# Optimization experiments

Hardware: AMD Instinct MI355X
Metric: run time of the kernel (lower is better)

The kernel has to match this reference:

```python
import jax, jax.numpy as jnp
import numpy as np

N = 262144      # nodes per graph
NC = 65536      # common nodes
D = 256         # feature_dim


def setup_inputs() -> dict:
    key = jax.random.key(0)
    ks = jax.random.split(key, 12)
    h_prop = jax.random.normal(ks[0], (N, D), dtype=jnp.float32)
    h_context = jax.random.normal(ks[1], (N, D), dtype=jnp.float32)
    h_orig = jax.random.normal(ks[2], (NC, D), dtype=jnp.float32)
    # unique indices (torch scatter-assign semantics are only well-defined without dups)
    idx_prop = jnp.sort(jax.random.permutation(ks[3], N)[:NC]).astype(jnp.int64)
    idx_ctx = jnp.sort(jax.random.permutation(ks[4], N)[:NC]).astype(jnp.int64)
    # parameters (xavier-ish scale)
    s = 1.0 / np.sqrt(D)
    w_orig = jax.random.normal(ks[5], (D, D), dtype=jnp.float32) * s
    w_prop = jax.random.normal(ks[6], (D, D), dtype=jnp.float32) * s
    w_ctx = jax.random.normal(ks[7], (D, D), dtype=jnp.float32) * s
    W_fuse = jax.random.normal(ks[8], (D, 3 * D), dtype=jnp.float32) * (1.0 / np.sqrt(3 * D))  # torch Linear weight (out,in)
    b_fuse = jnp.zeros((D,), dtype=jnp.float32)
    bias = jax.random.uniform(ks[9], (D,), dtype=jnp.float32, minval=-s, maxval=s)
    return {
        "h_prop": h_prop, "h_context": h_context,
        "h_original_common_nodes": h_orig,
        "w_orig": w_orig, "w_prop": w_prop, "w_ctx": w_ctx,
        "W_fuse": W_fuse, "b_fuse": b_fuse, "bias": bias,
        "common_node_indices_in_prop": idx_prop,
        "common_node_indices_in_context": idx_ctx,
    }


def reference(h_prop, h_context, h_original_common_nodes,
              w_orig, w_prop, w_ctx, W_fuse, b_fuse, bias,
              common_node_indices_in_prop, common_node_indices_in_context):
    # gather common rows + three small GEMMs  [NC, D]
    t_orig = h_original_common_nodes @ w_orig
    t_prop = h_prop[common_node_indices_in_prop] @ w_prop
    t_ctx = h_context[common_node_indices_in_context] @ w_ctx
    # concat-linear-tanh-bias  [NC, D]
    fused = jnp.concatenate([t_orig, t_prop, t_ctx], axis=1) @ W_fuse.T + b_fuse
    fused = jnp.tanh(fused) + bias
    # scatter update into clones of the full tables
    h_prop_updated = h_prop.at[common_node_indices_in_prop].set(fused)
    h_context_updated = h_context.at[common_node_indices_in_context].set(fused)
    return (h_prop_updated, h_context_updated)
```

## Files before the change

kernel.cpp:

```cpp
#include <hip/hip_runtime.h>
#include <hip/hip_bf16.h>
#include <math.h>

#define NN 262144
#define NCC 65536

typedef __bf16 bf16x8 __attribute__((ext_vector_type(8)));
typedef float f32x4 __attribute__((ext_vector_type(4)));

__global__ __launch_bounds__(256) void k_setup(const float* __restrict__ w_orig,
                                               const float* __restrict__ w_prop,
                                               const float* __restrict__ w_ctx,
                                               const float* __restrict__ W_fuse,
                                               __bf16* __restrict__ Mt,
                                               unsigned char* __restrict__ flags) {
    __shared__ float Wl[64 * 65];
    __shared__ float wl[64 * 65];
    int b = blockIdx.x;
    int t = threadIdx.x;
    if (b >= 48) {
        ((uint4*)flags)[(b - 48) * 256 + t] = make_uint4(0u, 0u, 0u, 0u);
        return;
    }
    int seg = b >> 4, rem = b & 15;
    int ot = rem >> 2, mt = rem & 3;
    const float* wseg = seg == 0 ? w_orig : (seg == 1 ? w_prop : w_ctx);
    int to = (t & 15) * 4, tm = (t >> 4) * 4;
    float acc[4][4] = {};
    for (int kc = 0; kc < 4; ++kc) {
        __syncthreads();
        for (int i = 0; i < 16; ++i) {
            int f = i * 256 + t;
            int row = f >> 6, col = f & 63;
            Wl[row * 65 + col] = W_fuse[(size_t)(ot * 64 + row) * 768 + seg * 256 + kc * 64 + col];
            wl[row * 65 + col] = wseg[(size_t)(mt * 64 + row) * 256 + kc * 64 + col];
        }
        __syncthreads();
        for (int k = 0; k < 64; ++k) {
            float wo[4], wm2[4];
#pragma unroll
            for (int i = 0; i < 4; ++i) wo[i] = Wl[(to + i) * 65 + k];
#pragma unroll
            for (int j = 0; j < 4; ++j) wm2[j] = wl[(tm + j) * 65 + k];
#pragma unroll
            for (int i = 0; i < 4; ++i)
#pragma unroll
                for (int j = 0; j < 4; ++j) acc[i][j] += wo[i] * wm2[j];
        }
    }
    for (int i = 0; i < 4; ++i)
        for (int j = 0; j < 4; ++j) {
            int o = ot * 64 + to + i;
            int g = seg * 256 + mt * 64 + tm + j;
            Mt[(size_t)o * 768 + g] = (__bf16)acc[i][j];
        }
}

__global__ void k_setflags(const int* __restrict__ idxp, const int* __restrict__ idxc,
                           unsigned char* fp, unsigned char* fc) {
    int j = blockIdx.x * blockDim.x + threadIdx.x;
    if (j < NCC) { fp[idxp[j]] = 1; fc[idxc[j]] = 1; }
}

__device__ inline bf16x8 cvt8(f32x4 a, f32x4 b) {
    bf16x8 w;
    w[0] = (__bf16)a[0]; w[1] = (__bf16)a[1]; w[2] = (__bf16)a[2]; w[3] = (__bf16)a[3];
    w[4] = (__bf16)b[0]; w[5] = (__bf16)b[1]; w[6] = (__bf16)b[2]; w[7] = (__bf16)b[3];
    return w;
}

__global__ __launch_bounds__(512, 4) void k_main(const float* __restrict__ hp,
                                                 const float* __restrict__ hc,
                                                 const float* __restrict__ horig,
                                                 const __bf16* __restrict__ Mt,
                                                 const float* __restrict__ bfuse,
                                                 const float* __restrict__ bias,
                                                 const int* __restrict__ idxp,
                                                 const int* __restrict__ idxc,
                                                 const unsigned char* __restrict__ fp,
                                                 const unsigned char* __restrict__ fc,
                                                 float* __restrict__ out0,
                                                 float* __restrict__ out1) {
    __shared__ char smem[40960];
    int bid = blockIdx.x >> 1;
    int t = threadIdx.x;

    if (!(blockIdx.x & 1)) {
        int tbl = bid >= 512;
        const unsigned char* F = tbl ? fc : fp;
        const float* S = tbl ? hc : hp;
        float* D = tbl ? out1 : out0;
        int r0 = (tbl ? bid - 512 : bid) * 512;
#pragma unroll
        for (int g = 0; g < 8; ++g) {
            unsigned char fl[8];
            f32x4 v[8];
#pragma unroll
            for (int i = 0; i < 8; ++i) {
                int gl = (g * 8 + i) * 512 + t;
                fl[i] = F[r0 + (gl >> 6)];
            }
#pragma unroll
            for (int i = 0; i < 8; ++i) {
                int gl = (g * 8 + i) * 512 + t;
                int r = r0 + (gl >> 6), slot = gl & 63;
                v[i] = *(const f32x4*)(S + (size_t)(fl[i] ? 0 : r) * 256 + slot * 4);
            }
#pragma unroll
            for (int i = 0; i < 8; ++i) {
                int gl = (g * 8 + i) * 512 + t;
                int r = r0 + (gl >> 6), slot = gl & 63;
                if (!fl[i]) *(f32x4*)(D + (size_t)r * 256 + slot * 4) = v[i];
            }
        }
        return;
    }

    __bf16* Al = (__bf16*)smem;
    __bf16* Bl = (__bf16*)(smem + 8192);
    int jbase = bid * 64;
    int lane = t & 63, wid = t >> 6;
    int wm = wid >> 2, wn = wid & 3;
    int l15 = lane & 15, lq = lane >> 4;

    int ar = t >> 3, aslot = t & 7;
    int jr = jbase + ar;
    const float* rowp0 = horig + (size_t)jr * 256 + aslot * 8;
    const float* rowp1 = hp + (size_t)idxp[jr] * 256 + aslot * 8;
    const float* rowp2 = hc + (size_t)idxc[jr] * 256 + aslot * 8;

    int bo = t >> 1, bkp = t & 1;
    const __bf16* bsrc = Mt + (size_t)bo * 768 + bkp * 32;

    f32x4 a0[2], a1[2];
    bf16x8 vb[4];
    {
        a0[0] = *(const f32x4*)(rowp0);       a1[0] = *(const f32x4*)(rowp0 + 4);
        a0[1] = *(const f32x4*)(rowp0 + 64);  a1[1] = *(const f32x4*)(rowp0 + 68);
#pragma unroll
        for (int i = 0; i < 4; ++i) vb[i] = *(const bf16x8*)(bsrc + i * 8);
    }

    f32x4 acc[2][4] = {};

#pragma unroll
    for (int c = 0; c < 12; ++c) {
        int s = c & 1;
        __syncthreads();
        *(bf16x8*)&Al[ar * 64 + ((aslot ^ (ar & 7)) << 3)] = cvt8(a0[s], a1[s]);
#pragma unroll
        for (int i = 0; i < 4; ++i) {
            int slot = bkp * 4 + i;
            *(bf16x8*)&Bl[bo * 64 + ((slot ^ (bo & 7)) << 3)] = vb[i];
        }
        if (c < 11) {
#pragma unroll
            for (int i = 0; i < 4; ++i) vb[i] = *(const bf16x8*)(bsrc + (c + 1) * 64 + i * 8);
        }
        if (c < 10) {
            int cn = c + 2;
            int seg = cn >> 2, ko = (cn & 3) * 64;
            const float* sp = (seg == 0 ? rowp0 : (seg == 1 ? rowp1 : rowp2)) + ko;
            a0[s] = *(const f32x4*)(sp);
            a1[s] = *(const f32x4*)(sp + 4);
        }
        __syncthreads();
#pragma unroll
        for (int ks = 0; ks < 2; ++ks) {
            bf16x8 af[2], bfr[4];
            int kslot = ks * 4 + lq;
#pragma unroll
            for (int mi = 0; mi < 2; ++mi) {
                int r = wm * 32 + mi * 16 + l15;
                af[mi] = *(const bf16x8*)&Al[r * 64 + ((kslot ^ (r & 7)) << 3)];
            }
#pragma unroll
            for (int ni = 0; ni < 4; ++ni) {
                int o = wn * 64 + ni * 16 + l15;
                bfr[ni] = *(const bf16x8*)&Bl[o * 64 + ((kslot ^ (o & 7)) << 3)];
            }
#pragma unroll
            for (int mi = 0; mi < 2; ++mi)
#pragma unroll
                for (int ni = 0; ni < 4; ++ni)
                    acc[mi][ni] = __builtin_amdgcn_mfma_f32_16x16x32_bf16(af[mi], bfr[ni], acc[mi][ni], 0, 0, 0);
        }
    }

    float bfv[4], biv[4];
#pragma unroll
    for (int ni = 0; ni < 4; ++ni) {
        int o = wn * 64 + ni * 16 + l15;
        bfv[ni] = bfuse[o];
        biv[ni] = bias[o];
    }
    __syncthreads();
    float* scr = (float*)(smem + 8192 + wid * 4096);
#pragma unroll
    for (int mi = 0; mi < 2; ++mi) {
#pragma unroll
        for (int ni = 0; ni < 4; ++ni)
#pragma unroll
            for (int rr = 0; rr < 4; ++rr) {
                float v = tanhf(acc[mi][ni][rr] + bfv[ni]) + biv[ni];
                scr[(lq * 4 + rr) * 64 + ni * 16 + l15] = v;
            }
#pragma unroll
        for (int rnd = 0; rnd < 4; ++rnd) {
            int rr2 = rnd * 4 + lq;
            int j = jbase + wm * 32 + mi * 16 + rr2;
            int gp = idxp[j], gc = idxc[j];
            f32x4 v = *(const f32x4*)&scr[rr2 * 64 + l15 * 4];
            *(f32x4*)(out0 + (size_t)gp * 256 + wn * 64 + l15 * 4) = v;
            *(f32x4*)(out1 + (size_t)gc * 256 + wn * 64 + l15 * 4) = v;
        }
    }
}

extern "C" void kernel_launch(void* const* d_in, const int* in_sizes, int n_in,
                              void* d_out, int out_size, void* d_ws, size_t ws_size,
                              hipStream_t stream) {
    const float* hp     = (const float*)d_in[0];
    const float* hc     = (const float*)d_in[1];
    const float* horig  = (const float*)d_in[2];
    const float* w_orig = (const float*)d_in[3];
    const float* w_prop = (const float*)d_in[4];
    const float* w_ctx  = (const float*)d_in[5];
    const float* W_fuse = (const float*)d_in[6];
    const float* bfuse  = (const float*)d_in[7];
    const float* bias   = (const float*)d_in[8];
    const int* idxp     = (const int*)d_in[9];
    const int* idxc     = (const int*)d_in[10];
    float* out0 = (float*)d_out;
    float* out1 = out0 + (size_t)NN * 256;

    char* ws = (char*)d_ws;
    __bf16* Mt = (__bf16*)ws;
    unsigned char* fp = (unsigned char*)(ws + 393216);
    unsigned char* fc = fp + NN;

    k_setup<<<176, 256, 0, stream>>>(w_orig, w_prop, w_ctx, W_fuse, Mt, fp);
    k_setflags<<<NCC / 256, 256, 0, stream>>>(idxp, idxc, fp, fc);
    k_main<<<2048, 512, 0, stream>>>(hp, hc, horig, Mt, bfuse, bias,
                                     idxp, idxc, fp, fc, out0, out1);
}
```

Before: 291.0 us.

## Split main kernel into streaming copy pass with bf16 compaction and GEMM pass

Replaces the per-row flag with a rank map, so a first streaming pass reads each table row once. It copies unmarked rows to the output and writes marked rows, converted to bf16, into a compact contiguous buffer. A second GEMM kernel then reads contiguous bf16 rows instead of random fp32 gathers from the large tables, and scatters the results. The aim is to remove the scattered gathers and halve the bytes the GEMM reads. The cost is an extra kernel launch, a serialization point between copy and GEMM, and about 64MB of extra bf16 workspace traffic.

```diff
diff --git a/kernel.cpp b/kernel.cpp
--- a/kernel.cpp
+++ b/kernel.cpp
@@ -6,6 +6,7 @@
 #define NCC 65536
 
 typedef __bf16 bf16x8 __attribute__((ext_vector_type(8)));
+typedef __bf16 bf16x4 __attribute__((ext_vector_type(4)));
 typedef float f32x4 __attribute__((ext_vector_type(4)));
 
 __global__ __launch_bounds__(256) void k_setup(const float* __restrict__ w_orig,
@@ -13,13 +14,13 @@
                                                const float* __restrict__ w_ctx,
                                                const float* __restrict__ W_fuse,
                                                __bf16* __restrict__ Mt,
-                                               unsigned char* __restrict__ flags) {
+                                               int* __restrict__ ranks) {
     __shared__ float Wl[64 * 65];
     __shared__ float wl[64 * 65];
     int b = blockIdx.x;
     int t = threadIdx.x;
     if (b >= 48) {
-        ((uint4*)flags)[(b - 48) * 256 + t] = make_uint4(0u, 0u, 0u, 0u);
+        ((uint4*)ranks)[(b - 48) * 256 + t] = make_uint4(0u, 0u, 0u, 0u);
         return;
     }
     int seg = b >> 4, rem = b & 15;
@@ -56,11 +57,53 @@
         }
 }
 
-__global__ void k_setflags(const int* __restrict__ idxp, const int* __restrict__ idxc,
-                           unsigned char* fp, unsigned char* fc) {
+__global__ void k_setrank(const int* __restrict__ idxp, const int* __restrict__ idxc,
+                          int* rankp, int* rankc) {
     int j = blockIdx.x * blockDim.x + threadIdx.x;
-    if (j < NCC) { fp[idxp[j]] = 1; fc[idxc[j]] = 1; }
-}
+    if (j < NCC) { rankp[idxp[j]] = j + 1; rankc[idxc[j]] = j + 1; }
+}
+
+__global__ __launch_bounds__(256) void k_pass1(const float* __restrict__ hp,
+                                               const float* __restrict__ hc,
+                                               const int* __restrict__ rankp,
+                                               const int* __restrict__ rankc,
+                                               __bf16* __restrict__ compP,
+                                               __bf16* __restrict__ compC,
+                                               float* __restrict__ out0,
+                                               float* __restrict__ out1) {
+    int bid = blockIdx.x;
+    int t = threadIdx.x, lane = t & 63, wid = t >> 6;
+    int tbl = bid >= 1024;
+    const float* S = tbl ? hc : hp;
+    const int* R = tbl ? rankc : rankp;
+    float* D = tbl ? out1 : out0;
+    __bf16* C = tbl ? compC : compP;
+    int r0 = (tbl ? bid - 1024 : bid) * 256 + wid * 64;
+#pragma unroll
+    for (int g = 0; g < 8; ++g) {
+        int rk[8];
+        f32x4 v[8];
+#pragma unroll
+        for (int i = 0; i < 8; ++i) rk[i] = R[r0 + g * 8 + i];
+#pragma unroll
+        for (int i = 0; i < 8; ++i)
+            v[i] = *(const f32x4*)(S + (size_t)(r0 + g * 8 + i) * 256 + lane * 4);
+#pragma unroll
+        for (int i = 0; i < 8; ++i) {
+            int r = r0 + g * 8 + i;
+            if (rk[i] == 0) {
+                *(f32x4*)(D + (size_t)r * 256 + lane * 4) = v[i];
+            } else {
+                bf16x4 w;
+                w[0] = (__bf16)v[i][0]; w[1] = (__bf16)v[i][1];
+                w[2] = (__bf16)v[i][2]; w[3] = (__bf16)v[i][3];
+                *(bf16x4*)(C + (size_t)(rk[i] - 1) * 256 + lane * 4) = w;
+            }
+        }
+    }
+}
+
+#define MFMA __builtin_amdgcn_mfma_f32_16x16x32_bf16
 
 __device__ inline bf16x8 cvt8(f32x4 a, f32x4 b) {
     bf16x8 w;
@@ -69,100 +112,64 @@
     return w;
 }
 
-__global__ __launch_bounds__(512, 4) void k_main(const float* __restrict__ hp,
-                                                 const float* __restrict__ hc,
-                                                 const float* __restrict__ horig,
-                                                 const __bf16* __restrict__ Mt,
-                                                 const float* __restrict__ bfuse,
-                                                 const float* __restrict__ bias,
-                                                 const int* __restrict__ idxp,
-                                                 const int* __restrict__ idxc,
-                                                 const unsigned char* __restrict__ fp,
-                                                 const unsigned char* __restrict__ fc,
-                                                 float* __restrict__ out0,
-                                                 float* __restrict__ out1) {
-    __shared__ char smem[40960];
-    int bid = blockIdx.x >> 1;
-    int t = threadIdx.x;
-
-    if (!(blockIdx.x & 1)) {
-        int tbl = bid >= 512;
-        const unsigned char* F = tbl ? fc : fp;
-        const float* S = tbl ? hc : hp;
-        float* D = tbl ? out1 : out0;
-        int r0 = (tbl ? bid - 512 : bid) * 512;
-#pragma unroll
-        for (int g = 0; g < 8; ++g) {
-            unsigned char fl[8];
-            f32x4 v[8];
-#pragma unroll
-            for (int i = 0; i < 8; ++i) {
-                int gl = (g * 8 + i) * 512 + t;
-                fl[i] = F[r0 + (gl >> 6)];
-            }
-#pragma unroll
-            for (int i = 0; i < 8; ++i) {
-                int gl = (g * 8 + i) * 512 + t;
-                int r = r0 + (gl >> 6), slot = gl & 63;
-                v[i] = *(const f32x4*)(S + (size_t)(fl[i] ? 0 : r) * 256 + slot * 4);
-            }
-#pragma unroll
-            for (int i = 0; i < 8; ++i) {
-                int gl = (g * 8 + i) * 512 + t;
-                int r = r0 + (gl >> 6), slot = gl & 63;
-                if (!fl[i]) *(f32x4*)(D + (size_t)r * 256 + slot * 4) = v[i];
-            }
-        }
-        return;
-    }
-
+__global__ __launch_bounds__(512, 4) void k_pass2(const float* __restrict__ horig,
+                                                  const __bf16* __restrict__ compP,
+                                                  const __bf16* __restrict__ compC,
+                                                  const __bf16* __restrict__ Mt,
+                                                  const float* __restrict__ bfuse,
+                                                  const float* __restrict__ bias,
+                                                  const int* __restrict__ idxp,
+                                                  const int* __restrict__ idxc,
+                                                  float* __restrict__ out0,
+                                                  float* __restrict__ out1) {
+    __shared__ __align__(16) char smem[40960];
     __bf16* Al = (__bf16*)smem;
     __bf16* Bl = (__bf16*)(smem + 8192);
-    int jbase = bid * 64;
+    int t = threadIdx.x;
+    int jbase = blockIdx.x * 64;
     int lane = t & 63, wid = t >> 6;
     int wm = wid >> 2, wn = wid & 3;
     int l15 = lane & 15, lq = lane >> 4;
 
     int ar = t >> 3, aslot = t & 7;
-    int jr = jbase + ar;
-    const float* rowp0 = horig + (size_t)jr * 256 + aslot * 8;
-    const float* rowp1 = hp + (size_t)idxp[jr] * 256 + aslot * 8;
-    const float* rowp2 = hc + (size_t)idxc[jr] * 256 + aslot * 8;
+    const float* arow0 = horig + (size_t)(jbase + ar) * 256 + aslot * 8;
+    const __bf16* arow1 = compP + (size_t)(jbase + ar) * 256 + aslot * 8;
+    const __bf16* arow2 = compC + (size_t)(jbase + ar) * 256 + aslot * 8;
 
     int bo = t >> 1, bkp = t & 1;
     const __bf16* bsrc = Mt + (size_t)bo * 768 + bkp * 32;
 
-    f32x4 a0[2], a1[2];
+    f32x4 acc[2][4] = {};
+
+    f32x4 va0 = *(const f32x4*)(arow0);
+    f32x4 va1 = *(const f32x4*)(arow0 + 4);
+    bf16x8 vab;
     bf16x8 vb[4];
-    {
-        a0[0] = *(const f32x4*)(rowp0);       a1[0] = *(const f32x4*)(rowp0 + 4);
-        a0[1] = *(const f32x4*)(rowp0 + 64);  a1[1] = *(const f32x4*)(rowp0 + 68);
-#pragma unroll
-        for (int i = 0; i < 4; ++i) vb[i] = *(const bf16x8*)(bsrc + i * 8);
-    }
-
-    f32x4 acc[2][4] = {};
+#pragma unroll
+    for (int i = 0; i < 4; ++i) vb[i] = *(const bf16x8*)(bsrc + i * 8);
 
 #pragma unroll
     for (int c = 0; c < 12; ++c) {
-        int s = c & 1;
-        __syncthreads();
-        *(bf16x8*)&Al[ar * 64 + ((aslot ^ (ar & 7)) << 3)] = cvt8(a0[s], a1[s]);
+        __syncthreads();
+        if (c < 4) *(bf16x8*)&Al[ar * 64 + ((aslot ^ (ar & 7)) << 3)] = cvt8(va0, va1);
+        else       *(bf16x8*)&Al[ar * 64 + ((aslot ^ (ar & 7)) << 3)] = vab;
 #pragma unroll
         for (int i = 0; i < 4; ++i) {
             int slot = bkp * 4 + i;
             *(bf16x8*)&Bl[bo * 64 + ((slot ^ (bo & 7)) << 3)] = vb[i];
         }
         if (c < 11) {
-#pragma unroll
-            for (int i = 0; i < 4; ++i) vb[i] = *(const bf16x8*)(bsrc + (c + 1) * 64 + i * 8);
-        }
-        if (c < 10) {
-            int cn = c + 2;
-            int seg = cn >> 2, ko = (cn & 3) * 64;
-            const float* sp = (seg == 0 ? rowp0 : (seg == 1 ? rowp1 : rowp2)) + ko;
-            a0[s] = *(const f32x4*)(sp);
-            a1[s] = *(const f32x4*)(sp + 4);
+            int cn = c + 1, ko = (cn & 3) * 64;
+            if (cn < 4) {
+                va0 = *(const f32x4*)(arow0 + ko);
+                va1 = *(const f32x4*)(arow0 + ko + 4);
+            } else if (cn < 8) {
+                vab = *(const bf16x8*)(arow1 + ko);
+            } else {
+                vab = *(const bf16x8*)(arow2 + ko);
+            }
+#pragma unroll
+            for (int i = 0; i < 4; ++i) vb[i] = *(const bf16x8*)(bsrc + cn * 64 + i * 8);
         }
         __syncthreads();
 #pragma unroll
@@ -183,7 +190,7 @@
             for (int mi = 0; mi < 2; ++mi)
 #pragma unroll
                 for (int ni = 0; ni < 4; ++ni)
-                    acc[mi][ni] = __builtin_amdgcn_mfma_f32_16x16x32_bf16(af[mi], bfr[ni], acc[mi][ni], 0, 0, 0);
+                    acc[mi][ni] = MFMA(af[mi], bfr[ni], acc[mi][ni], 0, 0, 0);
         }
     }
 
@@ -235,12 +242,15 @@
     float* out1 = out0 + (size_t)NN * 256;
 
     char* ws = (char*)d_ws;
-    __bf16* Mt = (__bf16*)ws;
-    unsigned char* fp = (unsigned char*)(ws + 393216);
-    unsigned char* fc = fp + NN;
-
-    k_setup<<<176, 256, 0, stream>>>(w_orig, w_prop, w_ctx, W_fuse, Mt, fp);
-    k_setflags<<<NCC / 256, 256, 0, stream>>>(idxp, idxc, fp, fc);
-    k_main<<<2048, 512, 0, stream>>>(hp, hc, horig, Mt, bfuse, bias,
-                                     idxp, idxc, fp, fc, out0, out1);
-}
+    __bf16* Mt  = (__bf16*)ws;
+    int* rankp  = (int*)(ws + 393216);
+    int* rankc  = (int*)(ws + 393216 + 1048576);
+    __bf16* compP = (__bf16*)(ws + 393216 + 2097152);
+    __bf16* compC = (__bf16*)(ws + 393216 + 2097152 + 33554432);
+
+    k_setup<<<560, 256, 0, stream>>>(w_orig, w_prop, w_ctx, W_fuse, Mt, rankp);
+    k_setrank<<<NCC / 256, 256, 0, stream>>>(idxp, idxc, rankp, rankc);
+    k_pass1<<<2048, 256, 0, stream>>>(hp, hc, rankp, rankc, compP, compC, out0, out1);
+    k_pass2<<<NCC / 64, 512, 0, stream>>>(horig, compP, compC, Mt, bfuse, bias,
+                                          idxp, idxc, out0, out1);
+}
```

Measured after the change: 346.3 us. 1.19x slower.
